# Kernel optimization log

Hardware: AMD Instinct MI355X
Metric: run time of the kernel (lower is better)

## Reference

```python
import jax, jax.numpy as jnp
import numpy as np

B, S, D, H = 1, 2048, 768, 12
HD = D // H


def layer_norm(x, g, b, eps=1e-5):
    mu = x.mean(-1, keepdims=True)
    var = ((x - mu) ** 2).mean(-1, keepdims=True)
    return (x - mu) * jax.lax.rsqrt(var + eps) * g + b


def setup_inputs() -> dict:
    key = jax.random.key(0)
    ks = jax.random.split(key, 16)
    s = 0.02
    exp_encodings = jax.random.normal(ks[0], (B, S, D), dtype=jnp.float32)
    pert_encodings = jax.random.normal(ks[1], (B, S, D), dtype=jnp.float32)
    adj = (jax.random.uniform(ks[2], (S, S)) < 0.01).astype(jnp.int32)
    adj = adj.at[jnp.arange(S), jnp.arange(S)].set(1)
    in_proj_w = jax.random.normal(ks[3], (3 * D, D)) * s
    in_proj_b = jnp.zeros((3 * D,), jnp.float32)
    out_proj_w = jax.random.normal(ks[4], (D, D)) * s
    out_proj_b = jnp.zeros((D,), jnp.float32)
    ln0_g = jnp.ones((D,), jnp.float32); ln0_b = jnp.zeros((D,), jnp.float32)
    ln1_g = jnp.ones((D,), jnp.float32); ln1_b = jnp.zeros((D,), jnp.float32)
    ln2_g = jnp.ones((D,), jnp.float32); ln2_b = jnp.zeros((D,), jnp.float32)
    w1 = jax.random.normal(ks[5], (D // 2, D)) * s
    b1 = jnp.zeros((D // 2,), jnp.float32)
    w2 = jax.random.normal(ks[6], (D, D // 2)) * s
    b2 = jnp.zeros((D,), jnp.float32)
    return dict(exp_encodings=exp_encodings, pert_encodings=pert_encodings,
                in_proj_w=in_proj_w, in_proj_b=in_proj_b,
                out_proj_w=out_proj_w, out_proj_b=out_proj_b,
                ln0_g=ln0_g, ln0_b=ln0_b, ln1_g=ln1_g, ln1_b=ln1_b,
                ln2_g=ln2_g, ln2_b=ln2_b, w1=w1, b1=b1, w2=w2, b2=b2,
                adj=adj)


def reference(exp_encodings, pert_encodings, in_proj_w, in_proj_b,
              out_proj_w, out_proj_b, ln0_g, ln0_b, ln1_g, ln1_b,
              ln2_g, ln2_b, w1, b1, w2, b2, adj):
    b, s, d = exp_encodings.shape
    hd = d // H
    # additive mask: 0 where edge, -inf elsewhere (diag guaranteed edge)
    mask = jnp.where(adj > 0, 0.0, -jnp.inf).astype(exp_encodings.dtype)
    x_in = layer_norm(exp_encodings + pert_encodings, ln0_g, ln0_b)
    # torch MultiheadAttention (batch_first) self-attention
    qkv = x_in @ in_proj_w.T + in_proj_b          # [b,s,3d]
    q, k, v = jnp.split(qkv, 3, axis=-1)
    q = q.reshape(b, s, H, hd)
    k = k.reshape(b, s, H, hd)
    v = v.reshape(b, s, H, hd)
    scores = jnp.einsum('bqhe,bkhe->bhqk', q, k) / np.sqrt(hd) + mask
    attn = jax.nn.softmax(scores, axis=-1)
    o = jnp.einsum('bhqk,bkhe->bqhe', attn, v).reshape(b, s, d)
    o = o @ out_proj_w.T + out_proj_b
    x = layer_norm(o + x_in, ln1_g, ln1_b)
    ff = jax.nn.relu(x @ w1.T + b1) @ w2.T + b2
    return layer_norm(x + ff, ln2_g, ln2_b)
```

## Files before the change

kernel.cpp:

```cpp
#include <hip/hip_runtime.h>

#define S 2048
#define D 768
#define NH 12
#define HD 64
#define TD (3 * D)

typedef __bf16 bf16_t;
typedef __bf16 v8bf __attribute__((ext_vector_type(8)));
typedef __bf16 v4bf __attribute__((ext_vector_type(4)));
typedef float v4f __attribute__((ext_vector_type(4)));

__device__ __forceinline__ float toF(float v) { return v; }
__device__ __forceinline__ float toF(bf16_t v) { return (float)v; }

__device__ __forceinline__ float wave_reduce_sum(float v) {
#pragma unroll
    for (int o = 32; o > 0; o >>= 1) v += __shfl_down(v, o, 64);
    return v;
}
__device__ float block_reduce_sum(float v) {
    __shared__ float t4[4];
    int lane = threadIdx.x & 63, wid = threadIdx.x >> 6;
    v = wave_reduce_sum(v);
    __syncthreads();
    if (lane == 0) t4[wid] = v;
    __syncthreads();
    return t4[0] + t4[1] + t4[2] + t4[3];
}

__global__ __launch_bounds__(256) void add_ln(const float* __restrict__ A, const float* __restrict__ Bv,
                                              const float* __restrict__ g, const float* __restrict__ be,
                                              bf16_t* __restrict__ out) {
    int row = blockIdx.x, t = threadIdx.x;
    const float* a = A + (size_t)row * D;
    const float* b = Bv + (size_t)row * D;
    float x[3];
    float s = 0.f;
#pragma unroll
    for (int i = 0; i < 3; ++i) { int c = t + 256 * i; x[i] = a[c] + b[c]; s += x[i]; }
    float mean = block_reduce_sum(s) * (1.0f / D);
    float vs = 0.f;
#pragma unroll
    for (int i = 0; i < 3; ++i) { float d = x[i] - mean; vs += d * d; }
    float var = block_reduce_sum(vs) * (1.0f / D);
    float rstd = rsqrtf(var + 1e-5f);
#pragma unroll
    for (int i = 0; i < 3; ++i) {
        int c = t + 256 * i;
        out[(size_t)row * D + c] = (bf16_t)((x[i] - mean) * rstd * g[c] + be[c]);
    }
}

template <typename TO>
__global__ __launch_bounds__(256) void ln_only(const bf16_t* __restrict__ X,
                                               const float* __restrict__ g, const float* __restrict__ be,
                                               TO* __restrict__ out) {
    int row = blockIdx.x, t = threadIdx.x;
    const bf16_t* a = X + (size_t)row * D;
    float x[3];
    float s = 0.f;
#pragma unroll
    for (int i = 0; i < 3; ++i) { int c = t + 256 * i; x[i] = (float)a[c]; s += x[i]; }
    float mean = block_reduce_sum(s) * (1.0f / D);
    float vs = 0.f;
#pragma unroll
    for (int i = 0; i < 3; ++i) { float d = x[i] - mean; vs += d * d; }
    float var = block_reduce_sum(vs) * (1.0f / D);
    float rstd = rsqrtf(var + 1e-5f);
#pragma unroll
    for (int i = 0; i < 3; ++i) {
        int c = t + 256 * i;
        out[(size_t)row * D + c] = (TO)((x[i] - mean) * rstd * g[c] + be[c]);
    }
}

#define NW0 (TD * D / 4)
#define NW1 (D * D / 4)
#define NW2 ((D / 2) * D / 4)
#define NW3 (D * (D / 2) / 4)
__global__ __launch_bounds__(256) void cvt_all(const float* __restrict__ s0, const float* __restrict__ s1,
                                               const float* __restrict__ s2, const float* __restrict__ s3,
                                               bf16_t* __restrict__ d0, bf16_t* __restrict__ d1,
                                               bf16_t* __restrict__ d2, bf16_t* __restrict__ d3) {
    int i = blockIdx.x * 256 + threadIdx.x;
    const float* sp; bf16_t* dp;
    if (i < NW0) { sp = s0; dp = d0; }
    else if (i < NW0 + NW1) { sp = s1; dp = d1; i -= NW0; }
    else if (i < NW0 + NW1 + NW2) { sp = s2; dp = d2; i -= NW0 + NW1; }
    else if (i < NW0 + NW1 + NW2 + NW3) { sp = s3; dp = d3; i -= NW0 + NW1 + NW2; }
    else return;
    float4 v = ((const float4*)sp)[i];
    v4bf o = {(bf16_t)v.x, (bf16_t)v.y, (bf16_t)v.z, (bf16_t)v.w};
    *(v4bf*)(dp + (size_t)i * 4) = o;
}

#define GBK 32

template <int TM, int TN, int RELU, bool RESID>
__global__ __launch_bounds__(256) void gemm_mfma(const bf16_t* __restrict__ A, const bf16_t* __restrict__ B,
                                                 const float* __restrict__ bias,
                                                 const bf16_t* __restrict__ Rsd, bf16_t* __restrict__ C,
                                                 int M, int N, int K) {
    constexpr int CA = TM * 4;
    constexpr int P = (TM + TN) / 64;
    constexpr int MI = TM / 32, NI = TN / 32;
    __shared__ bf16_t As[TM * GBK];
    __shared__ bf16_t Bs[TN * GBK];
    const int t = threadIdx.x;
    const int lane = t & 63, wave = t >> 6;
    const int wr = (wave >> 1) * (TM / 2), wc = (wave & 1) * (TN / 2);
    const int m0 = blockIdx.y * TM, n0 = blockIdx.x * TN;
    const int lm = lane & 15, q = lane >> 4;

    const bf16_t* gsrc[P];
    bf16_t* ldst[P];
#pragma unroll
    for (int p = 0; p < P; ++p) {
        int c = t + 256 * p;
        if (c < CA) {
            int row = c >> 2, col = (c & 3) * 8;
            gsrc[p] = A + (size_t)(m0 + row) * K + col;
            ldst[p] = As + c * 8;
        } else {
            int cc = c - CA;
            int row = cc >> 2, col = (cc & 3) * 8;
            gsrc[p] = B + (size_t)(n0 + row) * K + col;
            ldst[p] = Bs + cc * 8;
        }
    }

    v4f acc[MI][NI] = {};

    for (int k0 = 0; k0 < K; k0 += GBK) {
#pragma unroll
        for (int p = 0; p < P; ++p)
            __builtin_amdgcn_global_load_lds((const __attribute__((address_space(1))) void*)(gsrc[p] + k0),
                                             (__attribute__((address_space(3))) void*)ldst[p], 16, 0, 0);
        __syncthreads();

        v8bf af[MI], bfr[NI];
#pragma unroll
        for (int i = 0; i < MI; ++i) af[i] = *(const v8bf*)(As + (wr + i * 16 + lm) * GBK + q * 8);
#pragma unroll
        for (int j = 0; j < NI; ++j) bfr[j] = *(const v8bf*)(Bs + (wc + j * 16 + lm) * GBK + q * 8);
#pragma unroll
        for (int i = 0; i < MI; ++i)
#pragma unroll
            for (int j = 0; j < NI; ++j)
                acc[i][j] = __builtin_amdgcn_mfma_f32_16x16x32_bf16(af[i], bfr[j], acc[i][j], 0, 0, 0);
        __syncthreads();
    }

#pragma unroll
    for (int i = 0; i < MI; ++i)
#pragma unroll
        for (int j = 0; j < NI; ++j) {
            int col = n0 + wc + j * 16 + lm;
            float bs = bias[col];
#pragma unroll
            for (int r = 0; r < 4; ++r) {
                int row = m0 + wr + i * 16 + q * 4 + r;
                float v = acc[i][j][r] + bs;
                if (RELU) v = fmaxf(v, 0.f);
                if (RESID) v += (float)Rsd[(size_t)row * N + col];
                C[(size_t)row * N + col] = (bf16_t)v;
            }
        }
}

__global__ __launch_bounds__(256) void attn_sparse(const bf16_t* __restrict__ qkv, const int* __restrict__ adj,
                                                   bf16_t* __restrict__ O) {
    __shared__ int s_idx[128];
    __shared__ int s_cnt;
    __shared__ float s_q[D];
    __shared__ float s_p[NH][128];

    const int row = blockIdx.x, t = threadIdx.x;
    const int lane = t & 63, wave = t >> 6;
    if (t == 0) s_cnt = 0;
    __syncthreads();

    const int4* arow = (const int4*)(adj + (size_t)row * S);
#pragma unroll
    for (int p = 0; p < 2; ++p) {
        int4 v = arow[t + 256 * p];
        int base = (t + 256 * p) * 4;
        if (v.x) { int k = atomicAdd(&s_cnt, 1); if (k < 128) s_idx[k] = base + 0; }
        if (v.y) { int k = atomicAdd(&s_cnt, 1); if (k < 128) s_idx[k] = base + 1; }
        if (v.z) { int k = atomicAdd(&s_cnt, 1); if (k < 128) s_idx[k] = base + 2; }
        if (v.w) { int k = atomicAdd(&s_cnt, 1); if (k < 128) s_idx[k] = base + 3; }
    }
    for (int c = t; c < D; c += 256) s_q[c] = (float)qkv[(size_t)row * TD + c];
    __syncthreads();
    const int n = (s_cnt < 128) ? s_cnt : 128;

    for (int it = t; it < n * NH; it += 256) {
        int i = it / NH, h = it % NH;
        int j = s_idx[i];
        const bf16_t* kp = qkv + (size_t)j * TD + D + h * HD;
        const float* qp = s_q + h * HD;
        float dot = 0.f;
#pragma unroll
        for (int c = 0; c < HD; c += 8) {
            v8bf kv = *(const v8bf*)(kp + c);
#pragma unroll
            for (int e = 0; e < 8; ++e) dot += qp[c + e] * (float)kv[e];
        }
        s_p[h][i] = dot * 0.125f;
    }
    __syncthreads();

    for (int h = wave; h < NH; h += 4) {
        float v0 = (lane < n) ? s_p[h][lane] : -1e30f;
        float v1 = (lane + 64 < n) ? s_p[h][lane + 64] : -1e30f;
        float m = fmaxf(v0, v1);
#pragma unroll
        for (int o = 32; o > 0; o >>= 1) m = fmaxf(m, __shfl_xor(m, o, 64));
        float p0 = (lane < n) ? __expf(v0 - m) : 0.f;
        float p1 = (lane + 64 < n) ? __expf(v1 - m) : 0.f;
        float sm = p0 + p1;
#pragma unroll
        for (int o = 32; o > 0; o >>= 1) sm += __shfl_xor(sm, o, 64);
        float inv = 1.f / sm;
        if (lane < n) s_p[h][lane] = p0 * inv;
        if (lane + 64 < n) s_p[h][lane + 64] = p1 * inv;
    }
    __syncthreads();

    for (int o = t; o < D; o += 256) {
        int h = o >> 6, e = o & 63;
        const float* pp = s_p[h];
        float acc = 0.f;
        for (int i = 0; i < n; ++i)
            acc += pp[i] * (float)qkv[(size_t)s_idx[i] * TD + 2 * D + h * HD + e];
        O[(size_t)row * D + o] = (bf16_t)acc;
    }
}

extern "C" void kernel_launch(void* const* d_in, const int* in_sizes, int n_in,
                              void* d_out, int out_size, void* d_ws, size_t ws_size,
                              hipStream_t stream) {
    const float* exp_e = (const float*)d_in[0];
    const float* pert  = (const float*)d_in[1];
    const float* w_in  = (const float*)d_in[2];
    const float* b_in  = (const float*)d_in[3];
    const float* w_out = (const float*)d_in[4];
    const float* b_out = (const float*)d_in[5];
    const float* g0  = (const float*)d_in[6];
    const float* be0 = (const float*)d_in[7];
    const float* g1  = (const float*)d_in[8];
    const float* be1 = (const float*)d_in[9];
    const float* g2  = (const float*)d_in[10];
    const float* be2 = (const float*)d_in[11];
    const float* w1  = (const float*)d_in[12];
    const float* b1  = (const float*)d_in[13];
    const float* w2  = (const float*)d_in[14];
    const float* b2  = (const float*)d_in[15];
    const int*   adj = (const int*)d_in[16];
    float* out = (float*)d_out;

    const size_t SD = (size_t)S * D;
    bf16_t* wb_in  = (bf16_t*)d_ws;
    bf16_t* wb_out = wb_in + (size_t)TD * D;
    bf16_t* wb_1   = wb_out + (size_t)D * D;
    bf16_t* wb_2   = wb_1 + (size_t)(D / 2) * D;
    bf16_t* x_in   = wb_2 + (size_t)D * (D / 2);
    bf16_t* qkv    = x_in + SD;
    bf16_t* attn_o = qkv + 3 * SD;
    bf16_t* y1     = attn_o + SD;
    bf16_t* x1     = y1 + SD;
    bf16_t* ffh    = x1 + SD;
    bf16_t* y2     = ffh + SD / 2;

    const int NW = NW0 + NW1 + NW2 + NW3;
    cvt_all<<<(NW + 255) / 256, 256, 0, stream>>>(w_in, w_out, w1, w2, wb_in, wb_out, wb_1, wb_2);
    add_ln<<<S, 256, 0, stream>>>(exp_e, pert, g0, be0, x_in);
    gemm_mfma<64, 128, 0, false><<<dim3(TD / 128, S / 64), 256, 0, stream>>>(x_in, wb_in, b_in, nullptr, qkv, S, TD, D);
    attn_sparse<<<S, 256, 0, stream>>>(qkv, adj, attn_o);
    gemm_mfma<64, 64, 0, true><<<dim3(D / 64, S / 64), 256, 0, stream>>>(attn_o, wb_out, b_out, x_in, y1, S, D, D);
    ln_only<bf16_t><<<S, 256, 0, stream>>>(y1, g1, be1, x1);
    gemm_mfma<64, 64, 1, false><<<dim3((D / 2) / 64, S / 64), 256, 0, stream>>>(x1, wb_1, b1, nullptr, ffh, S, D / 2, D);
    gemm_mfma<64, 64, 0, true><<<dim3(D / 64, S / 64), 256, 0, stream>>>(ffh, wb_2, b2, x1, y2, S, D, D / 2);
    ln_only<float><<<S, 256, 0, stream>>>(y2, g2, be2, out);
}
```

Before: 204.2 us.

## Fuse weight conversion into add-LN, deepen GEMM K-step, retile FFN1 GEMM

Merges the weight-conversion kernel into the first add+layernorm launch as extra blocks, removing one kernel launch. GEMM K-tile doubles to 64, stored as two 32-wide slabs so each sync handles twice the MFMA work and half as many barriers run. The FFN1 GEMM uses 32x64 tiles for more blocks, and the attention score loop reorders its index mapping so consecutive threads share a head. Costs are higher LDS use per block and smaller tiles with less reuse in FFN1.

```diff
diff --git a/kernel.cpp b/kernel.cpp
--- a/kernel.cpp
+++ b/kernel.cpp
@@ -11,9 +11,6 @@
 typedef __bf16 v4bf __attribute__((ext_vector_type(4)));
 typedef float v4f __attribute__((ext_vector_type(4)));
 
-__device__ __forceinline__ float toF(float v) { return v; }
-__device__ __forceinline__ float toF(bf16_t v) { return (float)v; }
-
 __device__ __forceinline__ float wave_reduce_sum(float v) {
 #pragma unroll
     for (int o = 32; o > 0; o >>= 1) v += __shfl_down(v, o, 64);
@@ -29,10 +26,34 @@
     return t4[0] + t4[1] + t4[2] + t4[3];
 }
 
-__global__ __launch_bounds__(256) void add_ln(const float* __restrict__ A, const float* __restrict__ Bv,
-                                              const float* __restrict__ g, const float* __restrict__ be,
-                                              bf16_t* __restrict__ out) {
-    int row = blockIdx.x, t = threadIdx.x;
+#define NW0 (TD * D / 4)
+#define NW1 (D * D / 4)
+#define NW2 ((D / 2) * D / 4)
+#define NW3 (D * (D / 2) / 4)
+#define NWALL (NW0 + NW1 + NW2 + NW3)
+
+__global__ __launch_bounds__(256) void addln_cvt(const float* __restrict__ A, const float* __restrict__ Bv,
+                                                 const float* __restrict__ g, const float* __restrict__ be,
+                                                 bf16_t* __restrict__ out,
+                                                 const float* __restrict__ s0, const float* __restrict__ s1,
+                                                 const float* __restrict__ s2, const float* __restrict__ s3,
+                                                 bf16_t* __restrict__ d0, bf16_t* __restrict__ d1,
+                                                 bf16_t* __restrict__ d2, bf16_t* __restrict__ d3) {
+    int blk = blockIdx.x, t = threadIdx.x;
+    if (blk >= S) {
+        int i = (blk - S) * 256 + t;
+        const float* sp; bf16_t* dp;
+        if (i < NW0) { sp = s0; dp = d0; }
+        else if (i < NW0 + NW1) { sp = s1; dp = d1; i -= NW0; }
+        else if (i < NW0 + NW1 + NW2) { sp = s2; dp = d2; i -= NW0 + NW1; }
+        else if (i < NWALL) { sp = s3; dp = d3; i -= NW0 + NW1 + NW2; }
+        else return;
+        float4 v = ((const float4*)sp)[i];
+        v4bf o = {(bf16_t)v.x, (bf16_t)v.y, (bf16_t)v.z, (bf16_t)v.w};
+        *(v4bf*)(dp + (size_t)i * 4) = o;
+        return;
+    }
+    int row = blk;
     const float* a = A + (size_t)row * D;
     const float* b = Bv + (size_t)row * D;
     float x[3];
@@ -75,35 +96,17 @@
     }
 }
 
-#define NW0 (TD * D / 4)
-#define NW1 (D * D / 4)
-#define NW2 ((D / 2) * D / 4)
-#define NW3 (D * (D / 2) / 4)
-__global__ __launch_bounds__(256) void cvt_all(const float* __restrict__ s0, const float* __restrict__ s1,
-                                               const float* __restrict__ s2, const float* __restrict__ s3,
-                                               bf16_t* __restrict__ d0, bf16_t* __restrict__ d1,
-                                               bf16_t* __restrict__ d2, bf16_t* __restrict__ d3) {
-    int i = blockIdx.x * 256 + threadIdx.x;
-    const float* sp; bf16_t* dp;
-    if (i < NW0) { sp = s0; dp = d0; }
-    else if (i < NW0 + NW1) { sp = s1; dp = d1; i -= NW0; }
-    else if (i < NW0 + NW1 + NW2) { sp = s2; dp = d2; i -= NW0 + NW1; }
-    else if (i < NW0 + NW1 + NW2 + NW3) { sp = s3; dp = d3; i -= NW0 + NW1 + NW2; }
-    else return;
-    float4 v = ((const float4*)sp)[i];
-    v4bf o = {(bf16_t)v.x, (bf16_t)v.y, (bf16_t)v.z, (bf16_t)v.w};
-    *(v4bf*)(dp + (size_t)i * 4) = o;
-}
-
-#define GBK 32
+#define GBK 64
 
 template <int TM, int TN, int RELU, bool RESID>
 __global__ __launch_bounds__(256) void gemm_mfma(const bf16_t* __restrict__ A, const bf16_t* __restrict__ B,
                                                  const float* __restrict__ bias,
                                                  const bf16_t* __restrict__ Rsd, bf16_t* __restrict__ C,
                                                  int M, int N, int K) {
-    constexpr int CA = TM * 4;
-    constexpr int P = (TM + TN) / 64;
+    constexpr int CA = TM * 8;
+    constexpr int CHUNKS = (TM + TN) * 8;
+    constexpr int P = CHUNKS / 256;
+    static_assert(CHUNKS % 256 == 0, "chunk passes must be exact");
     constexpr int MI = TM / 32, NI = TN / 32;
     __shared__ bf16_t As[TM * GBK];
     __shared__ bf16_t Bs[TN * GBK];
@@ -119,14 +122,16 @@
     for (int p = 0; p < P; ++p) {
         int c = t + 256 * p;
         if (c < CA) {
-            int row = c >> 2, col = (c & 3) * 8;
-            gsrc[p] = A + (size_t)(m0 + row) * K + col;
-            ldst[p] = As + c * 8;
+            int slab = c / (TM * 4), r4 = c % (TM * 4);
+            int row = r4 >> 2, c4 = r4 & 3;
+            gsrc[p] = A + (size_t)(m0 + row) * K + slab * 32 + c4 * 8;
+            ldst[p] = As + slab * (TM * 32) + row * 32 + c4 * 8;
         } else {
             int cc = c - CA;
-            int row = cc >> 2, col = (cc & 3) * 8;
-            gsrc[p] = B + (size_t)(n0 + row) * K + col;
-            ldst[p] = Bs + cc * 8;
+            int slab = cc / (TN * 4), r4 = cc % (TN * 4);
+            int row = r4 >> 2, c4 = r4 & 3;
+            gsrc[p] = B + (size_t)(n0 + row) * K + slab * 32 + c4 * 8;
+            ldst[p] = Bs + slab * (TN * 32) + row * 32 + c4 * 8;
         }
     }
 
@@ -139,16 +144,23 @@
                                              (__attribute__((address_space(3))) void*)ldst[p], 16, 0, 0);
         __syncthreads();
 
-        v8bf af[MI], bfr[NI];
-#pragma unroll
-        for (int i = 0; i < MI; ++i) af[i] = *(const v8bf*)(As + (wr + i * 16 + lm) * GBK + q * 8);
-#pragma unroll
-        for (int j = 0; j < NI; ++j) bfr[j] = *(const v8bf*)(Bs + (wc + j * 16 + lm) * GBK + q * 8);
-#pragma unroll
-        for (int i = 0; i < MI; ++i)
+        v8bf af[2][MI], bfr[2][NI];
+#pragma unroll
+        for (int s = 0; s < 2; ++s) {
+#pragma unroll
+            for (int i = 0; i < MI; ++i)
+                af[s][i] = *(const v8bf*)(As + s * (TM * 32) + (wr + i * 16 + lm) * 32 + q * 8);
 #pragma unroll
             for (int j = 0; j < NI; ++j)
-                acc[i][j] = __builtin_amdgcn_mfma_f32_16x16x32_bf16(af[i], bfr[j], acc[i][j], 0, 0, 0);
+                bfr[s][j] = *(const v8bf*)(Bs + s * (TN * 32) + (wc + j * 16 + lm) * 32 + q * 8);
+        }
+#pragma unroll
+        for (int s = 0; s < 2; ++s)
+#pragma unroll
+            for (int i = 0; i < MI; ++i)
+#pragma unroll
+                for (int j = 0; j < NI; ++j)
+                    acc[i][j] = __builtin_amdgcn_mfma_f32_16x16x32_bf16(af[s][i], bfr[s][j], acc[i][j], 0, 0, 0);
         __syncthreads();
     }
 
@@ -196,7 +208,7 @@
     const int n = (s_cnt < 128) ? s_cnt : 128;
 
     for (int it = t; it < n * NH; it += 256) {
-        int i = it / NH, h = it % NH;
+        int h = it / n, i = it - h * n;
         int j = s_idx[i];
         const bf16_t* kp = qkv + (size_t)j * TD + D + h * HD;
         const float* qp = s_q + h * HD;
@@ -273,14 +285,14 @@
     bf16_t* ffh    = x1 + SD;
     bf16_t* y2     = ffh + SD / 2;
 
-    const int NW = NW0 + NW1 + NW2 + NW3;
-    cvt_all<<<(NW + 255) / 256, 256, 0, stream>>>(w_in, w_out, w1, w2, wb_in, wb_out, wb_1, wb_2);
-    add_ln<<<S, 256, 0, stream>>>(exp_e, pert, g0, be0, x_in);
+    const int CVTB = (NWALL + 255) / 256;
+    addln_cvt<<<S + CVTB, 256, 0, stream>>>(exp_e, pert, g0, be0, x_in,
+                                            w_in, w_out, w1, w2, wb_in, wb_out, wb_1, wb_2);
     gemm_mfma<64, 128, 0, false><<<dim3(TD / 128, S / 64), 256, 0, stream>>>(x_in, wb_in, b_in, nullptr, qkv, S, TD, D);
     attn_sparse<<<S, 256, 0, stream>>>(qkv, adj, attn_o);
     gemm_mfma<64, 64, 0, true><<<dim3(D / 64, S / 64), 256, 0, stream>>>(attn_o, wb_out, b_out, x_in, y1, S, D, D);
     ln_only<bf16_t><<<S, 256, 0, stream>>>(y1, g1, be1, x1);
-    gemm_mfma<64, 64, 1, false><<<dim3((D / 2) / 64, S / 64), 256, 0, stream>>>(x1, wb_1, b1, nullptr, ffh, S, D / 2, D);
+    gemm_mfma<32, 64, 1, false><<<dim3((D / 2) / 64, S / 32), 256, 0, stream>>>(x1, wb_1, b1, nullptr, ffh, S, D / 2, D);
     gemm_mfma<64, 64, 0, true><<<dim3(D / 64, S / 64), 256, 0, stream>>>(ffh, wb_2, b2, x1, y2, S, D, D / 2);
     ln_only<float><<<S, 256, 0, stream>>>(y2, g2, be2, out);
 }
```

After: 196.3 us. 1.04x faster.
